# Performance work log

Hardware: AMD Instinct MI355X
Metric: run time of the kernel (lower is better)

## Reference

```python
import jax, jax.numpy as jnp
import numpy as np

D = 256          # input_dim (node embedding dim)
ATT_TIMES = 2
ATT_NUM = 2
DIN = D * ATT_NUM  # NTN input dim = 512
F = 16           # feature_map_dim


def setup_inputs() -> dict:
    key = jax.random.key(0)
    ks = jax.random.split(key, 10)
    x1 = jax.random.normal(ks[0], (120000, D), dtype=jnp.float32)
    x2 = jax.random.normal(ks[1], (100000, D), dtype=jnp.float32)
    # attention weight (glorot)
    W0 = jax.random.normal(ks[2], (D, D), dtype=jnp.float32) * (2.0 / (D + D)) ** 0.5
    # NTN params
    V = jax.random.normal(ks[3], (F, 2 * DIN), dtype=jnp.float32) * (2.0 / (F + 2 * DIN)) ** 0.5
    W = jax.random.normal(ks[4], (F, DIN, DIN), dtype=jnp.float32) * (2.0 / (DIN + DIN)) ** 0.5
    b = jax.random.normal(ks[5], (F,), dtype=jnp.float32)
    # projection MLP 16->8->4->2->1, torch Linear weights are (out, in)
    P0 = jax.random.normal(ks[6], (8, 16), dtype=jnp.float32) * (2.0 / (8 + 16)) ** 0.5
    P1 = jax.random.normal(ks[7], (4, 8), dtype=jnp.float32) * (2.0 / (4 + 8)) ** 0.5
    P2 = jax.random.normal(ks[8], (2, 4), dtype=jnp.float32) * (2.0 / (2 + 4)) ** 0.5
    P3 = jax.random.normal(ks[9], (1, 2), dtype=jnp.float32) * (2.0 / (1 + 2)) ** 0.5
    return {"x1": x1, "x2": x2, "W0": W0, "V": V, "W": W, "b": b,
            "P0": P0, "P1": P1, "P2": P2, "P3": P3}


def _attention(x, W0):
    # x: (N, D) -> (1, D*ATT_NUM) graph embedding.
    outs = []
    for _ in range(ATT_NUM):  # 'dot' style: same params each head (eye W), kept for faithfulness
        cur = x
        out = None
        for _ in range(ATT_TIMES):
            temp = jnp.mean(cur, axis=0, keepdims=True)          # (1, D)
            h_avg = jnp.tanh(temp @ W0)                          # att_weight=True
            att = jax.nn.sigmoid(cur @ h_avg.T)                  # (N, 1), W=eye in 'dot' style
            out = att.T @ cur                                    # (1, D)
            cur = cur * att
        outs.append(out)
    return jnp.concatenate(outs, axis=1)                         # (1, DIN)


def _ntn(g1, g2, V, W, b):
    # g1, g2: (1, DIN). Fused bilinear over all F feature maps.
    concat = jnp.concatenate([g1, g2], axis=1)                   # (1, 2*DIN)
    v_term = concat @ V.T                                        # (1, F)
    w_term = jnp.einsum('nd,fde,me->nf', g1, W, g2)              # (1, F)
    return jax.nn.sigmoid(v_term + w_term + b)                   # inneract = sigmoid


def reference(x1, x2, W0, V, W, b, P0, P1, P2, P3):
    g1 = _attention(x1, W0)
    g2 = _attention(x2, W0)
    x = _ntn(g1, g2, V, W, b)                                    # (1, F), branch 'an'
    for P in (P0, P1, P2, P3):                                   # Linear(no bias) + Sigmoid
        x = jax.nn.sigmoid(x @ P.T)
    return x                                                     # (1, 1)
```

## Files before the change

kernel.cpp:

```cpp
#include <hip/hip_runtime.h>
#include <math.h>

#define DD 256
#define REPS 8

#define OFF_SUMREP 0
#define OFF_H1P    4096
#define OFF_S1REP  4608
#define OFF_H2P    8704
#define OFF_OREP   9216
#define OFF_O      13312
#define OFF_WTREP  13824
#define WS_FLOATS  13952

__device__ __forceinline__ float sigmoidf_(float x) { return 1.0f / (1.0f + __expf(-x)); }
__device__ __forceinline__ float dot4(float4 a, float4 b) {
    return a.x * b.x + a.y * b.y + a.z * b.z + a.w * b.w;
}
__device__ __forceinline__ void fma4(float4& acc, float s, float4 v) {
    acc.x += s * v.x; acc.y += s * v.y; acc.z += s * v.z; acc.w += s * v.w;
}
__device__ __forceinline__ void add4(float4& acc, float4 v) {
    acc.x += v.x; acc.y += v.y; acc.z += v.z; acc.w += v.w;
}
__device__ __forceinline__ float wave_sum(float v) {
#pragma unroll
    for (int off = 32; off; off >>= 1) v += __shfl_xor(v, off, 64);
    return v;
}

__global__ void k_zero(float* __restrict__ ws) {
    int i = blockIdx.x * 256 + threadIdx.x;
    if (i < WS_FLOATS) ws[i] = 0.0f;
}

__device__ __forceinline__ void block_reduce_atomic(float4 acc, int t, float* dst_base) {
    __shared__ float4 lds[256];
    lds[t] = acc;
    __syncthreads();
    if (t < 64) {
        float4 s = lds[t];
        add4(s, lds[t + 64]); add4(s, lds[t + 128]); add4(s, lds[t + 192]);
        float* dst = dst_base + t * 4;
        atomicAdd(dst + 0, s.x); atomicAdd(dst + 1, s.y);
        atomicAdd(dst + 2, s.z); atomicAdd(dst + 3, s.w);
    }
}

__global__ void __launch_bounds__(256, 4)
k_mean(const float* __restrict__ x1, const float* __restrict__ x2,
       int N1, int N2, float* __restrict__ ws) {
    int b = blockIdx.x, t = threadIdx.x;
    int inp = b >> 10;
    int bl = b & 1023;
    const float4* x = (const float4*)(inp ? x2 : x1);
    int N = inp ? N2 : N1;
    int chunk = (N + 1023) >> 10;
    int start = bl * chunk;
    int end = min(start + chunk, N);
    int lane = t & 63, w = t >> 6;
    float4 a0 = make_float4(0.f, 0.f, 0.f, 0.f), a1 = a0;
    int r = start + w;
    for (; r + 28 < end; r += 32) {
        const float4* p = x + (size_t)r * 64 + lane;
        float4 v[8];
#pragma unroll
        for (int u = 0; u < 8; u++) v[u] = p[u * 256];
#pragma unroll
        for (int u = 0; u < 8; u += 2) { add4(a0, v[u]); add4(a1, v[u + 1]); }
    }
    for (; r < end; r += 4) add4(a0, x[(size_t)r * 64 + lane]);
    add4(a0, a1);
    block_reduce_atomic(a0, t, ws + OFF_SUMREP + inp * (REPS * 256) + (bl & (REPS - 1)) * 256);
}

__global__ void k_hpart(const float* __restrict__ W0, float* __restrict__ ws,
                        int srcOff, int dstOff, int N1, int N2) {
    int inp = blockIdx.x >> 4, g = blockIdx.x & 15;
    int t = threadIdx.x;
    __shared__ float temp[16];
    if (t < 16) {
        const float* src = ws + srcOff + inp * (REPS * 256) + g * 16 + t;
        float s = 0.f;
#pragma unroll
        for (int r = 0; r < REPS; r++) s += src[r * 256];
        temp[t] = s * (1.0f / (float)(inp ? N2 : N1));
    }
    __syncthreads();
    float p = 0.f;
#pragma unroll
    for (int j = 0; j < 16; j++) p += temp[j] * W0[(g * 16 + j) * 256 + t];
    atomicAdd(ws + dstOff + inp * 256 + t, p);
}

__global__ void __launch_bounds__(256, 4)
k_att1(const float* __restrict__ x1, const float* __restrict__ x2,
       int N1, int N2, float* __restrict__ ws) {
    int b = blockIdx.x, t = threadIdx.x;
    int inp = b >> 10;
    int bl = b & 1023;
    const float4* x = (const float4*)(inp ? x2 : x1);
    int N = inp ? N2 : N1;
    int chunk = (N + 1023) >> 10;
    int start = bl * chunk;
    int end = min(start + chunk, N);
    int lane = t & 63, w = t >> 6;
    float4 hp = ((const float4*)(ws + OFF_H1P + inp * 256))[lane];
    float4 h1 = make_float4(tanhf(hp.x), tanhf(hp.y), tanhf(hp.z), tanhf(hp.w));
    float4 acc = make_float4(0.f, 0.f, 0.f, 0.f);
    int r = start + w;
    for (; r + 28 < end; r += 32) {
        const float4* p = x + (size_t)r * 64 + lane;
        float4 v[8];
#pragma unroll
        for (int u = 0; u < 8; u++) v[u] = p[u * 256];
        float d[8];
#pragma unroll
        for (int u = 0; u < 8; u++) d[u] = dot4(v[u], h1);
#pragma unroll
        for (int off = 32; off; off >>= 1) {
#pragma unroll
            for (int u = 0; u < 8; u++) d[u] += __shfl_xor(d[u], off, 64);
        }
#pragma unroll
        for (int u = 0; u < 8; u++) fma4(acc, sigmoidf_(d[u]), v[u]);
    }
    for (; r < end; r += 4) {
        float4 v = x[(size_t)r * 64 + lane];
        float d = wave_sum(dot4(v, h1));
        fma4(acc, sigmoidf_(d), v);
    }
    block_reduce_atomic(acc, t, ws + OFF_S1REP + inp * (REPS * 256) + (bl & (REPS - 1)) * 256);
}

__global__ void __launch_bounds__(256, 4)
k_att2(const float* __restrict__ x1, const float* __restrict__ x2,
       int N1, int N2, float* __restrict__ ws) {
    int b = blockIdx.x, t = threadIdx.x;
    int inp = b >> 10;
    int bl = b & 1023;
    const float4* x = (const float4*)(inp ? x2 : x1);
    int N = inp ? N2 : N1;
    int chunk = (N + 1023) >> 10;
    int start = bl * chunk;
    int end = min(start + chunk, N);
    int lane = t & 63, w = t >> 6;
    float4 hp1 = ((const float4*)(ws + OFF_H1P + inp * 256))[lane];
    float4 hp2 = ((const float4*)(ws + OFF_H2P + inp * 256))[lane];
    float4 h1 = make_float4(tanhf(hp1.x), tanhf(hp1.y), tanhf(hp1.z), tanhf(hp1.w));
    float4 h2 = make_float4(tanhf(hp2.x), tanhf(hp2.y), tanhf(hp2.z), tanhf(hp2.w));
    float4 acc = make_float4(0.f, 0.f, 0.f, 0.f);
    int r = start + w;
    for (; r + 28 < end; r += 32) {
        const float4* p = x + (size_t)r * 64 + lane;
        float4 v[8];
#pragma unroll
        for (int u = 0; u < 8; u++) v[u] = p[u * 256];
        float d[8], e[8];
#pragma unroll
        for (int u = 0; u < 8; u++) { d[u] = dot4(v[u], h1); e[u] = dot4(v[u], h2); }
#pragma unroll
        for (int off = 32; off; off >>= 1) {
#pragma unroll
            for (int u = 0; u < 8; u++) {
                d[u] += __shfl_xor(d[u], off, 64);
                e[u] += __shfl_xor(e[u], off, 64);
            }
        }
#pragma unroll
        for (int u = 0; u < 8; u++) {
            float a1 = sigmoidf_(d[u]);
            fma4(acc, a1 * sigmoidf_(a1 * e[u]), v[u]);
        }
    }
    for (; r < end; r += 4) {
        float4 v = x[(size_t)r * 64 + lane];
        float d = dot4(v, h1), e = dot4(v, h2);
#pragma unroll
        for (int off = 32; off; off >>= 1) {
            d += __shfl_xor(d, off, 64); e += __shfl_xor(e, off, 64);
        }
        float a1 = sigmoidf_(d);
        fma4(acc, a1 * sigmoidf_(a1 * e), v);
    }
    block_reduce_atomic(acc, t, ws + OFF_OREP + inp * (REPS * 256) + (bl & (REPS - 1)) * 256);
}

__global__ void k_comb(float* __restrict__ ws) {
    int t = threadIdx.x;
    int inp = t >> 8, c = t & 255;
    float s = 0.f;
#pragma unroll
    for (int r = 0; r < REPS; r++) s += ws[OFF_OREP + inp * (REPS * 256) + r * 256 + c];
    ws[OFF_O + t] = s;
}

__global__ void __launch_bounds__(256, 4)
k_ntn(const float* __restrict__ W, float* __restrict__ ws) {
    int b = blockIdx.x, t = threadIdx.x;
    int lane = t & 63, w = t >> 6;
    const float* o1 = ws + OFF_O;
    float4 o2f = ((const float4*)(ws + OFF_O + 256))[lane];
    int f = b >> 5;
    int r0 = b * 16 + w;
    const float4* W4 = (const float4*)W;
    const float4* q0 = W4 + (size_t)r0 * 128 + lane;
    float4 va[8];
#pragma unroll
    for (int u = 0; u < 4; u++) { va[2 * u] = q0[u * 512]; va[2 * u + 1] = q0[u * 512 + 64]; }
    float p0 = (va[0].x + va[1].x) * o2f.x + (va[0].y + va[1].y) * o2f.y
             + (va[0].z + va[1].z) * o2f.z + (va[0].w + va[1].w) * o2f.w;
    float p1 = (va[2].x + va[3].x) * o2f.x + (va[2].y + va[3].y) * o2f.y
             + (va[2].z + va[3].z) * o2f.z + (va[2].w + va[3].w) * o2f.w;
    float p2 = (va[4].x + va[5].x) * o2f.x + (va[4].y + va[5].y) * o2f.y
             + (va[4].z + va[5].z) * o2f.z + (va[4].w + va[5].w) * o2f.w;
    float p3 = (va[6].x + va[7].x) * o2f.x + (va[6].y + va[7].y) * o2f.y
             + (va[6].z + va[7].z) * o2f.z + (va[6].w + va[7].w) * o2f.w;
#pragma unroll
    for (int off = 32; off; off >>= 1) {
        p0 += __shfl_xor(p0, off, 64); p1 += __shfl_xor(p1, off, 64);
        p2 += __shfl_xor(p2, off, 64); p3 += __shfl_xor(p3, off, 64);
    }
    if (lane == 0) {
        float* dst = ws + OFF_WTREP + (b & (REPS - 1)) * 16 + f;
        int d = r0 & 511;
        atomicAdd(dst, o1[d & 255] * p0
                     + o1[(d + 4) & 255] * p1
                     + o1[(d + 8) & 255] * p2
                     + o1[(d + 12) & 255] * p3);
    }
}

__global__ void k_final(const float* __restrict__ V, const float* __restrict__ bb,
                        const float* __restrict__ P0, const float* __restrict__ P1,
                        const float* __restrict__ P2, const float* __restrict__ P3,
                        float* __restrict__ ws, float* __restrict__ out) {
    int t = threadIdx.x;
    const float* o = ws + OFF_O;
    int f = t >> 4, j = t & 15;
    float p = 0.f;
    for (int k = j; k < 1024; k += 16) {
        float cv = (k < 512) ? o[k & 255] : o[256 + (k & 255)];
        p += cv * V[f * 1024 + k];
    }
    __shared__ float red[256];
    __shared__ float sv[16];
    red[t] = p;
    __syncthreads();
    if (t < 16) {
        float v = 0.f;
#pragma unroll
        for (int q = 0; q < 16; q++) v += red[t * 16 + q];
        float wt = 0.f;
#pragma unroll
        for (int r = 0; r < REPS; r++) wt += ws[OFF_WTREP + r * 16 + t];
        sv[t] = sigmoidf_(v + wt + bb[t]);
    }
    __syncthreads();
    if (t == 0) {
        float y0[8], y1[4], y2[2];
#pragma unroll
        for (int i = 0; i < 8; i++) {
            float s = 0.f;
            for (int k = 0; k < 16; k++) s += P0[i * 16 + k] * sv[k];
            y0[i] = sigmoidf_(s);
        }
#pragma unroll
        for (int i = 0; i < 4; i++) {
            float s = 0.f;
            for (int k = 0; k < 8; k++) s += P1[i * 8 + k] * y0[k];
            y1[i] = sigmoidf_(s);
        }
#pragma unroll
        for (int i = 0; i < 2; i++) {
            float s = 0.f;
            for (int k = 0; k < 4; k++) s += P2[i * 4 + k] * y1[k];
            y2[i] = sigmoidf_(s);
        }
        out[0] = sigmoidf_(P3[0] * y2[0] + P3[1] * y2[1]);
    }
}

extern "C" void kernel_launch(void* const* d_in, const int* in_sizes, int n_in,
                              void* d_out, int out_size, void* d_ws, size_t ws_size,
                              hipStream_t stream) {
    const float* x1 = (const float*)d_in[0];
    const float* x2 = (const float*)d_in[1];
    const float* W0 = (const float*)d_in[2];
    const float* V  = (const float*)d_in[3];
    const float* W  = (const float*)d_in[4];
    const float* b  = (const float*)d_in[5];
    const float* P0 = (const float*)d_in[6];
    const float* P1 = (const float*)d_in[7];
    const float* P2 = (const float*)d_in[8];
    const float* P3 = (const float*)d_in[9];
    float* ws  = (float*)d_ws;
    float* out = (float*)d_out;
    int N1 = in_sizes[0] / DD;
    int N2 = in_sizes[1] / DD;

    k_zero  <<<55,   256, 0, stream>>>(ws);
    k_mean  <<<2048, 256, 0, stream>>>(x1, x2, N1, N2, ws);
    k_hpart <<<32,   256, 0, stream>>>(W0, ws, OFF_SUMREP, OFF_H1P, N1, N2);
    k_att1  <<<2048, 256, 0, stream>>>(x1, x2, N1, N2, ws);
    k_hpart <<<32,   256, 0, stream>>>(W0, ws, OFF_S1REP, OFF_H2P, N1, N2);
    k_att2  <<<2048, 256, 0, stream>>>(x1, x2, N1, N2, ws);
    k_comb  <<<1,    512, 0, stream>>>(ws);
    k_ntn   <<<512,  256, 0, stream>>>(W, ws);
    k_final <<<1,    256, 0, stream>>>(V, b, P0, P1, P2, P3, ws, out);
}
```

Baseline: 407.8 us.

## Use grid-strided sweeps over both inputs and reshape NTN row mapping

The mean and attention kernels stop giving each block a contiguous chunk of rows from one input. Instead 1024 blocks sweep both x1 and x2 with a grid stride, so every pass reads addresses spread across the whole array, using ext_vector float4 arithmetic and a smaller unroll. The NTN kernel now maps each wave to four rows spaced 2048 apart, each with its own wave reduction and atomic, instead of four nearby rows. The aim is a more even and coalesced DRAM access pattern with less per-thread register state. The cost is lower memory-level parallelism per thread and more atomics in the NTN kernel.

```diff
diff --git a/kernel.cpp b/kernel.cpp
--- a/kernel.cpp
+++ b/kernel.cpp
@@ -13,15 +13,18 @@
 #define OFF_WTREP  13824
 #define WS_FLOATS  13952
 
+#define SWEEP_BLOCKS 1024
+#define SWEEP_W ((size_t)SWEEP_BLOCKS * 256)
+
+typedef float f32x4 __attribute__((ext_vector_type(4)));
+
 __device__ __forceinline__ float sigmoidf_(float x) { return 1.0f / (1.0f + __expf(-x)); }
-__device__ __forceinline__ float dot4(float4 a, float4 b) {
+__device__ __forceinline__ float dot4(f32x4 a, f32x4 b) {
     return a.x * b.x + a.y * b.y + a.z * b.z + a.w * b.w;
 }
-__device__ __forceinline__ void fma4(float4& acc, float s, float4 v) {
-    acc.x += s * v.x; acc.y += s * v.y; acc.z += s * v.z; acc.w += s * v.w;
-}
-__device__ __forceinline__ void add4(float4& acc, float4 v) {
-    acc.x += v.x; acc.y += v.y; acc.z += v.z; acc.w += v.w;
+__device__ __forceinline__ f32x4 tanh4(f32x4 a) {
+    f32x4 r; r.x = tanhf(a.x); r.y = tanhf(a.y); r.z = tanhf(a.z); r.w = tanhf(a.w);
+    return r;
 }
 __device__ __forceinline__ float wave_sum(float v) {
 #pragma unroll
@@ -34,44 +37,44 @@
     if (i < WS_FLOATS) ws[i] = 0.0f;
 }
 
-__device__ __forceinline__ void block_reduce_atomic(float4 acc, int t, float* dst_base) {
-    __shared__ float4 lds[256];
+__device__ __forceinline__ void block_reduce_atomic(f32x4 acc, int t, float* dst_base,
+                                                    f32x4* lds) {
     lds[t] = acc;
     __syncthreads();
     if (t < 64) {
-        float4 s = lds[t];
-        add4(s, lds[t + 64]); add4(s, lds[t + 128]); add4(s, lds[t + 192]);
+        f32x4 s = lds[t] + lds[t + 64] + lds[t + 128] + lds[t + 192];
         float* dst = dst_base + t * 4;
         atomicAdd(dst + 0, s.x); atomicAdd(dst + 1, s.y);
         atomicAdd(dst + 2, s.z); atomicAdd(dst + 3, s.w);
     }
+    __syncthreads();
 }
 
 __global__ void __launch_bounds__(256, 4)
 k_mean(const float* __restrict__ x1, const float* __restrict__ x2,
        int N1, int N2, float* __restrict__ ws) {
-    int b = blockIdx.x, t = threadIdx.x;
-    int inp = b >> 10;
-    int bl = b & 1023;
-    const float4* x = (const float4*)(inp ? x2 : x1);
-    int N = inp ? N2 : N1;
-    int chunk = (N + 1023) >> 10;
-    int start = bl * chunk;
-    int end = min(start + chunk, N);
-    int lane = t & 63, w = t >> 6;
-    float4 a0 = make_float4(0.f, 0.f, 0.f, 0.f), a1 = a0;
-    int r = start + w;
-    for (; r + 28 < end; r += 32) {
-        const float4* p = x + (size_t)r * 64 + lane;
-        float4 v[8];
-#pragma unroll
-        for (int u = 0; u < 8; u++) v[u] = p[u * 256];
-#pragma unroll
-        for (int u = 0; u < 8; u += 2) { add4(a0, v[u]); add4(a1, v[u + 1]); }
-    }
-    for (; r < end; r += 4) add4(a0, x[(size_t)r * 64 + lane]);
-    add4(a0, a1);
-    block_reduce_atomic(a0, t, ws + OFF_SUMREP + inp * (REPS * 256) + (bl & (REPS - 1)) * 256);
+    int t = threadIdx.x;
+    size_t idx = (size_t)blockIdx.x * 256 + t;
+    const f32x4* p1 = (const f32x4*)x1;
+    const f32x4* p2 = (const f32x4*)x2;
+    size_t end1 = (size_t)N1 * 64, end2 = (size_t)N2 * 64;
+    f32x4 a = {0.f, 0.f, 0.f, 0.f}, b = a;
+    size_t i = idx;
+    for (; i + 3 * SWEEP_W < end1; i += 4 * SWEEP_W) {
+        f32x4 v0 = p1[i], v1 = p1[i + SWEEP_W], v2 = p1[i + 2 * SWEEP_W], v3 = p1[i + 3 * SWEEP_W];
+        a += (v0 + v1) + (v2 + v3);
+    }
+    for (; i < end1; i += SWEEP_W) a += p1[i];
+    i = idx;
+    for (; i + 3 * SWEEP_W < end2; i += 4 * SWEEP_W) {
+        f32x4 v0 = p2[i], v1 = p2[i + SWEEP_W], v2 = p2[i + 2 * SWEEP_W], v3 = p2[i + 3 * SWEEP_W];
+        b += (v0 + v1) + (v2 + v3);
+    }
+    for (; i < end2; i += SWEEP_W) b += p2[i];
+    __shared__ f32x4 lds[256];
+    int rep = blockIdx.x & (REPS - 1);
+    block_reduce_atomic(a, t, ws + OFF_SUMREP + rep * 256, lds);
+    block_reduce_atomic(b, t, ws + OFF_SUMREP + (REPS + rep) * 256, lds);
 }
 
 __global__ void k_hpart(const float* __restrict__ W0, float* __restrict__ ws,
@@ -96,94 +99,113 @@
 __global__ void __launch_bounds__(256, 4)
 k_att1(const float* __restrict__ x1, const float* __restrict__ x2,
        int N1, int N2, float* __restrict__ ws) {
-    int b = blockIdx.x, t = threadIdx.x;
-    int inp = b >> 10;
-    int bl = b & 1023;
-    const float4* x = (const float4*)(inp ? x2 : x1);
-    int N = inp ? N2 : N1;
-    int chunk = (N + 1023) >> 10;
-    int start = bl * chunk;
-    int end = min(start + chunk, N);
-    int lane = t & 63, w = t >> 6;
-    float4 hp = ((const float4*)(ws + OFF_H1P + inp * 256))[lane];
-    float4 h1 = make_float4(tanhf(hp.x), tanhf(hp.y), tanhf(hp.z), tanhf(hp.w));
-    float4 acc = make_float4(0.f, 0.f, 0.f, 0.f);
-    int r = start + w;
-    for (; r + 28 < end; r += 32) {
-        const float4* p = x + (size_t)r * 64 + lane;
-        float4 v[8];
-#pragma unroll
-        for (int u = 0; u < 8; u++) v[u] = p[u * 256];
-        float d[8];
-#pragma unroll
-        for (int u = 0; u < 8; u++) d[u] = dot4(v[u], h1);
-#pragma unroll
-        for (int off = 32; off; off >>= 1) {
-#pragma unroll
-            for (int u = 0; u < 8; u++) d[u] += __shfl_xor(d[u], off, 64);
-        }
-#pragma unroll
-        for (int u = 0; u < 8; u++) fma4(acc, sigmoidf_(d[u]), v[u]);
-    }
-    for (; r < end; r += 4) {
-        float4 v = x[(size_t)r * 64 + lane];
-        float d = wave_sum(dot4(v, h1));
-        fma4(acc, sigmoidf_(d), v);
-    }
-    block_reduce_atomic(acc, t, ws + OFF_S1REP + inp * (REPS * 256) + (bl & (REPS - 1)) * 256);
+    int t = threadIdx.x;
+    int lane = t & 63;
+    size_t idx = (size_t)blockIdx.x * 256 + t;
+    const f32x4* p1 = (const f32x4*)x1;
+    const f32x4* p2 = (const f32x4*)x2;
+    size_t end1 = (size_t)N1 * 64, end2 = (size_t)N2 * 64;
+    f32x4 hA = tanh4(((const f32x4*)(ws + OFF_H1P))[lane]);
+    f32x4 hB = tanh4(((const f32x4*)(ws + OFF_H1P + 256))[lane]);
+    f32x4 accA = {0.f, 0.f, 0.f, 0.f}, accB = accA;
+    size_t i = idx;
+    for (; i + SWEEP_W < end1; i += 2 * SWEEP_W) {
+        f32x4 v0 = p1[i], v1 = p1[i + SWEEP_W];
+        float d0 = dot4(v0, hA), d1 = dot4(v1, hA);
+#pragma unroll
+        for (int off = 32; off; off >>= 1) {
+            d0 += __shfl_xor(d0, off, 64); d1 += __shfl_xor(d1, off, 64);
+        }
+        accA += sigmoidf_(d0) * v0 + sigmoidf_(d1) * v1;
+    }
+    for (; i < end1; i += SWEEP_W) {
+        f32x4 v = p1[i];
+        accA += sigmoidf_(wave_sum(dot4(v, hA))) * v;
+    }
+    i = idx;
+    for (; i + SWEEP_W < end2; i += 2 * SWEEP_W) {
+        f32x4 v0 = p2[i], v1 = p2[i + SWEEP_W];
+        float d0 = dot4(v0, hB), d1 = dot4(v1, hB);
+#pragma unroll
+        for (int off = 32; off; off >>= 1) {
+            d0 += __shfl_xor(d0, off, 64); d1 += __shfl_xor(d1, off, 64);
+        }
+        accB += sigmoidf_(d0) * v0 + sigmoidf_(d1) * v1;
+    }
+    for (; i < end2; i += SWEEP_W) {
+        f32x4 v = p2[i];
+        accB += sigmoidf_(wave_sum(dot4(v, hB))) * v;
+    }
+    __shared__ f32x4 lds[256];
+    int rep = blockIdx.x & (REPS - 1);
+    block_reduce_atomic(accA, t, ws + OFF_S1REP + rep * 256, lds);
+    block_reduce_atomic(accB, t, ws + OFF_S1REP + (REPS + rep) * 256, lds);
 }
 
 __global__ void __launch_bounds__(256, 4)
 k_att2(const float* __restrict__ x1, const float* __restrict__ x2,
        int N1, int N2, float* __restrict__ ws) {
-    int b = blockIdx.x, t = threadIdx.x;
-    int inp = b >> 10;
-    int bl = b & 1023;
-    const float4* x = (const float4*)(inp ? x2 : x1);
-    int N = inp ? N2 : N1;
-    int chunk = (N + 1023) >> 10;
-    int start = bl * chunk;
-    int end = min(start + chunk, N);
-    int lane = t & 63, w = t >> 6;
-    float4 hp1 = ((const float4*)(ws + OFF_H1P + inp * 256))[lane];
-    float4 hp2 = ((const float4*)(ws + OFF_H2P + inp * 256))[lane];
-    float4 h1 = make_float4(tanhf(hp1.x), tanhf(hp1.y), tanhf(hp1.z), tanhf(hp1.w));
-    float4 h2 = make_float4(tanhf(hp2.x), tanhf(hp2.y), tanhf(hp2.z), tanhf(hp2.w));
-    float4 acc = make_float4(0.f, 0.f, 0.f, 0.f);
-    int r = start + w;
-    for (; r + 28 < end; r += 32) {
-        const float4* p = x + (size_t)r * 64 + lane;
-        float4 v[8];
-#pragma unroll
-        for (int u = 0; u < 8; u++) v[u] = p[u * 256];
-        float d[8], e[8];
-#pragma unroll
-        for (int u = 0; u < 8; u++) { d[u] = dot4(v[u], h1); e[u] = dot4(v[u], h2); }
-#pragma unroll
-        for (int off = 32; off; off >>= 1) {
-#pragma unroll
-            for (int u = 0; u < 8; u++) {
-                d[u] += __shfl_xor(d[u], off, 64);
-                e[u] += __shfl_xor(e[u], off, 64);
-            }
-        }
-#pragma unroll
-        for (int u = 0; u < 8; u++) {
-            float a1 = sigmoidf_(d[u]);
-            fma4(acc, a1 * sigmoidf_(a1 * e[u]), v[u]);
-        }
-    }
-    for (; r < end; r += 4) {
-        float4 v = x[(size_t)r * 64 + lane];
-        float d = dot4(v, h1), e = dot4(v, h2);
+    int t = threadIdx.x;
+    int lane = t & 63;
+    size_t idx = (size_t)blockIdx.x * 256 + t;
+    const f32x4* p1 = (const f32x4*)x1;
+    const f32x4* p2 = (const f32x4*)x2;
+    size_t end1 = (size_t)N1 * 64, end2 = (size_t)N2 * 64;
+    f32x4 h1A = tanh4(((const f32x4*)(ws + OFF_H1P))[lane]);
+    f32x4 h1B = tanh4(((const f32x4*)(ws + OFF_H1P + 256))[lane]);
+    f32x4 h2A = tanh4(((const f32x4*)(ws + OFF_H2P))[lane]);
+    f32x4 h2B = tanh4(((const f32x4*)(ws + OFF_H2P + 256))[lane]);
+    f32x4 accA = {0.f, 0.f, 0.f, 0.f}, accB = accA;
+    size_t i = idx;
+    for (; i + SWEEP_W < end1; i += 2 * SWEEP_W) {
+        f32x4 v0 = p1[i], v1 = p1[i + SWEEP_W];
+        float d0 = dot4(v0, h1A), d1 = dot4(v1, h1A);
+        float e0 = dot4(v0, h2A), e1 = dot4(v1, h2A);
+#pragma unroll
+        for (int off = 32; off; off >>= 1) {
+            d0 += __shfl_xor(d0, off, 64); e0 += __shfl_xor(e0, off, 64);
+            d1 += __shfl_xor(d1, off, 64); e1 += __shfl_xor(e1, off, 64);
+        }
+        float a0 = sigmoidf_(d0), a1 = sigmoidf_(d1);
+        accA += (a0 * sigmoidf_(a0 * e0)) * v0 + (a1 * sigmoidf_(a1 * e1)) * v1;
+    }
+    for (; i < end1; i += SWEEP_W) {
+        f32x4 v = p1[i];
+        float d = dot4(v, h1A), e = dot4(v, h2A);
 #pragma unroll
         for (int off = 32; off; off >>= 1) {
             d += __shfl_xor(d, off, 64); e += __shfl_xor(e, off, 64);
         }
         float a1 = sigmoidf_(d);
-        fma4(acc, a1 * sigmoidf_(a1 * e), v);
-    }
-    block_reduce_atomic(acc, t, ws + OFF_OREP + inp * (REPS * 256) + (bl & (REPS - 1)) * 256);
+        accA += (a1 * sigmoidf_(a1 * e)) * v;
+    }
+    i = idx;
+    for (; i + SWEEP_W < end2; i += 2 * SWEEP_W) {
+        f32x4 v0 = p2[i], v1 = p2[i + SWEEP_W];
+        float d0 = dot4(v0, h1B), d1 = dot4(v1, h1B);
+        float e0 = dot4(v0, h2B), e1 = dot4(v1, h2B);
+#pragma unroll
+        for (int off = 32; off; off >>= 1) {
+            d0 += __shfl_xor(d0, off, 64); e0 += __shfl_xor(e0, off, 64);
+            d1 += __shfl_xor(d1, off, 64); e1 += __shfl_xor(e1, off, 64);
+        }
+        float a0 = sigmoidf_(d0), a1 = sigmoidf_(d1);
+        accB += (a0 * sigmoidf_(a0 * e0)) * v0 + (a1 * sigmoidf_(a1 * e1)) * v1;
+    }
+    for (; i < end2; i += SWEEP_W) {
+        f32x4 v = p2[i];
+        float d = dot4(v, h1B), e = dot4(v, h2B);
+#pragma unroll
+        for (int off = 32; off; off >>= 1) {
+            d += __shfl_xor(d, off, 64); e += __shfl_xor(e, off, 64);
+        }
+        float a1 = sigmoidf_(d);
+        accB += (a1 * sigmoidf_(a1 * e)) * v;
+    }
+    __shared__ f32x4 lds[256];
+    int rep = blockIdx.x & (REPS - 1);
+    block_reduce_atomic(accA, t, ws + OFF_OREP + rep * 256, lds);
+    block_reduce_atomic(accB, t, ws + OFF_OREP + (REPS + rep) * 256, lds);
 }
 
 __global__ void k_comb(float* __restrict__ ws) {
@@ -200,34 +222,25 @@
     int b = blockIdx.x, t = threadIdx.x;
     int lane = t & 63, w = t >> 6;
     const float* o1 = ws + OFF_O;
-    float4 o2f = ((const float4*)(ws + OFF_O + 256))[lane];
-    int f = b >> 5;
-    int r0 = b * 16 + w;
-    const float4* W4 = (const float4*)W;
-    const float4* q0 = W4 + (size_t)r0 * 128 + lane;
-    float4 va[8];
-#pragma unroll
-    for (int u = 0; u < 4; u++) { va[2 * u] = q0[u * 512]; va[2 * u + 1] = q0[u * 512 + 64]; }
-    float p0 = (va[0].x + va[1].x) * o2f.x + (va[0].y + va[1].y) * o2f.y
-             + (va[0].z + va[1].z) * o2f.z + (va[0].w + va[1].w) * o2f.w;
-    float p1 = (va[2].x + va[3].x) * o2f.x + (va[2].y + va[3].y) * o2f.y
-             + (va[2].z + va[3].z) * o2f.z + (va[2].w + va[3].w) * o2f.w;
-    float p2 = (va[4].x + va[5].x) * o2f.x + (va[4].y + va[5].y) * o2f.y
-             + (va[4].z + va[5].z) * o2f.z + (va[4].w + va[5].w) * o2f.w;
-    float p3 = (va[6].x + va[7].x) * o2f.x + (va[6].y + va[7].y) * o2f.y
-             + (va[6].z + va[7].z) * o2f.z + (va[6].w + va[7].w) * o2f.w;
-#pragma unroll
-    for (int off = 32; off; off >>= 1) {
-        p0 += __shfl_xor(p0, off, 64); p1 += __shfl_xor(p1, off, 64);
-        p2 += __shfl_xor(p2, off, 64); p3 += __shfl_xor(p3, off, 64);
+    f32x4 o2f = ((const f32x4*)(ws + OFF_O + 256))[lane];
+    int g = b * 4 + w;
+    const f32x4* W4 = (const f32x4*)W;
+    float wt[4];
+    int fidx[4];
+#pragma unroll
+    for (int u = 0; u < 4; u++) {
+        int row = g + u * 2048;
+        const f32x4* q = W4 + (size_t)row * 128 + lane;
+        f32x4 a = q[0], c = q[64];
+        float p = dot4(a + c, o2f);
+        p = wave_sum(p);
+        wt[u] = o1[row & 255] * p;
+        fidx[u] = row >> 9;
     }
     if (lane == 0) {
-        float* dst = ws + OFF_WTREP + (b & (REPS - 1)) * 16 + f;
-        int d = r0 & 511;
-        atomicAdd(dst, o1[d & 255] * p0
-                     + o1[(d + 4) & 255] * p1
-                     + o1[(d + 8) & 255] * p2
-                     + o1[(d + 12) & 255] * p3);
+        float* dst = ws + OFF_WTREP + (b & (REPS - 1)) * 16;
+#pragma unroll
+        for (int u = 0; u < 4; u++) atomicAdd(dst + fidx[u], wt[u]);
     }
 }
 
@@ -299,13 +312,13 @@
     int N1 = in_sizes[0] / DD;
     int N2 = in_sizes[1] / DD;
 
-    k_zero  <<<55,   256, 0, stream>>>(ws);
-    k_mean  <<<2048, 256, 0, stream>>>(x1, x2, N1, N2, ws);
-    k_hpart <<<32,   256, 0, stream>>>(W0, ws, OFF_SUMREP, OFF_H1P, N1, N2);
-    k_att1  <<<2048, 256, 0, stream>>>(x1, x2, N1, N2, ws);
-    k_hpart <<<32,   256, 0, stream>>>(W0, ws, OFF_S1REP, OFF_H2P, N1, N2);
-    k_att2  <<<2048, 256, 0, stream>>>(x1, x2, N1, N2, ws);
-    k_comb  <<<1,    512, 0, stream>>>(ws);
-    k_ntn   <<<512,  256, 0, stream>>>(W, ws);
-    k_final <<<1,    256, 0, stream>>>(V, b, P0, P1, P2, P3, ws, out);
-}
+    k_zero  <<<55,           256, 0, stream>>>(ws);
+    k_mean  <<<SWEEP_BLOCKS, 256, 0, stream>>>(x1, x2, N1, N2, ws);
+    k_hpart <<<32,           256, 0, stream>>>(W0, ws, OFF_SUMREP, OFF_H1P, N1, N2);
+    k_att1  <<<SWEEP_BLOCKS, 256, 0, stream>>>(x1, x2, N1, N2, ws);
+    k_hpart <<<32,           256, 0, stream>>>(W0, ws, OFF_S1REP, OFF_H2P, N1, N2);
+    k_att2  <<<SWEEP_BLOCKS, 256, 0, stream>>>(x1, x2, N1, N2, ws);
+    k_comb  <<<1,            512, 0, stream>>>(ws);
+    k_ntn   <<<512,          256, 0, stream>>>(W, ws);
+    k_final <<<1,            256, 0, stream>>>(V, b, P0, P1, P2, P3, ws, out);
+}
```

After: 433.1 us. 6.2% more time.
